# Kernel tuning notes

Measured on AMD Instinct MI355X. Metric: run time of the kernel, lower is better.

The kernel has to match this reference:

```python
import jax, jax.numpy as jnp
import numpy as np

QMIN, QMAX = -128, 127  # int8 range


def _quantize(x, scale, zero_point):
    """Affine quantize float -> int8: clamp(round(x/scale) + zp, -128, 127)."""
    q = jnp.round(x / scale) + zero_point
    return jnp.clip(q, QMIN, QMAX).astype(jnp.int8)


def setup_inputs() -> dict:
    key = jax.random.key(0)
    k1, k2, k3 = jax.random.split(key, 3)
    N, IN, OUT = 8192, 4096, 4096
    inp = jax.random.normal(k1, (N, IN), dtype=jnp.float32)
    # int8 weight table [OUT, IN]
    weight = jax.random.randint(k2, (OUT, IN), QMIN, QMAX + 1, dtype=jnp.int32).astype(jnp.int8)
    # int32 bias [OUT]
    bias = jax.random.randint(k3, (OUT,), -(2 ** 15), 2 ** 15, dtype=jnp.int32)
    return {
        "input": inp,
        "weight": weight,
        "bias": bias,
        "input_scale": 0.02,
        "input_zero_point": 0,
        "output_scale": 4096.0,
        "output_zero_point": 0,
    }


def reference(input, weight, bias, input_scale, input_zero_point, output_scale, output_zero_point):
    # 1) affine quantize input to int8
    q_input = _quantize(input, input_scale, input_zero_point)
    # 2) int32 matmul: F.linear(q_input.int32, weight.int32, bias.int32)
    acc = jnp.matmul(q_input.astype(jnp.int32), weight.astype(jnp.int32).T) + bias  # [N, OUT] int32
    # 3) requantize int32 accumulator to int8 with output scale/zero-point
    q_output = _quantize(acc.astype(jnp.float32), output_scale, output_zero_point)
    return q_output
```

## Files before the change

kernel.cpp:

```cpp
#include <hip/hip_runtime.h>
#include <stdint.h>

typedef int v4i __attribute__((ext_vector_type(4)));
typedef int v16i __attribute__((ext_vector_type(16)));

__device__ __forceinline__ int clamp_i8(int v) {
    return v < -128 ? -128 : (v > 127 ? 127 : v);
}

__device__ __forceinline__ void async_load16(const void* g, void* l) {
    __builtin_amdgcn_global_load_lds(
        (const __attribute__((address_space(1))) void*)g,
        (__attribute__((address_space(3))) void*)l, 16, 0, 0);
}

__global__ void quant_input_kernel(const float4* __restrict__ x, int* __restrict__ q,
                                   const float* __restrict__ scale_p,
                                   const int* __restrict__ zp_p, int n4) {
    const float inv = 1.0f / *scale_p;
    const int zp = *zp_p;
    const int stride = gridDim.x * blockDim.x;
    for (int t = blockIdx.x * blockDim.x + threadIdx.x; t < n4; t += stride) {
        float4 v = x[t];
        int q0 = clamp_i8((int)rintf(v.x * inv) + zp);
        int q1 = clamp_i8((int)rintf(v.y * inv) + zp);
        int q2 = clamp_i8((int)rintf(v.z * inv) + zp);
        int q3 = clamp_i8((int)rintf(v.w * inv) + zp);
        q[t] = (q0 & 255) | ((q1 & 255) << 8) | ((q2 & 255) << 16) | ((q3 & 255) << 24);
    }
}

__global__ void pack_weight_kernel(const int* __restrict__ w, int4* __restrict__ q,
                                   int K, int nfrag) {
    const int stride = gridDim.x * blockDim.x;
    const int Kc32 = K / 32;
    for (int t = blockIdx.x * blockDim.x + threadIdx.x; t < nfrag; t += stride) {
        const int l = t & 63;
        const int rest = t >> 6;
        const int k32 = rest % Kc32;
        const int c32 = rest / Kc32;
        const int col = c32 * 32 + (l & 31);
        const int kb = k32 * 32 + (l >> 5) * 16;
        const int* src = w + (int64_t)col * K + kb;
        int4 out;
        int* op = (int*)&out;
#pragma unroll
        for (int j = 0; j < 4; j++) {
            int4 v = *(const int4*)(src + 4 * j);
            op[j] = (v.x & 255) | ((v.y & 255) << 8) | ((v.z & 255) << 16) | ((v.w & 255) << 24);
        }
        q[t] = out;
    }
}

#define BM 256
#define BN 128
#define BK 64

__global__ __launch_bounds__(256, 2) void gemm_i8_kernel(
    const int8_t* __restrict__ A, const int8_t* __restrict__ W,
    const int* __restrict__ bias, int* __restrict__ C,
    const float* __restrict__ oscale_p, const int* __restrict__ ozp_p,
    int N, int K, int M) {
    __shared__ int8_t lA[2][BM * BK];

    const int tid = threadIdx.x;
    const int lane = tid & 63;
    const int w = tid >> 6;
    const int wm = w >> 1;
    const int wn = w & 1;

    const int bm = blockIdx.y * BM;
    const int bn = blockIdx.x * BN;

    const int s_sub = lane >> 2;
    const int s_col = (((lane & 3) ^ ((s_sub >> 1) & 3))) * 16;
    const int8_t* gA = A + (int64_t)(bm + w * 64 + s_sub) * K + s_col;
    const int64_t rs = (int64_t)16 * K;
    int8_t* lA0 = &lA[0][w * 4096];
    int8_t* lA1 = &lA[1][w * 4096];

    const int Kc32 = K >> 5;
    const int8_t* pB = W + ((int64_t)(blockIdx.x * (BN / 32) + wn * 2) * Kc32 * 64 +
                            lane) * 16;
    const int64_t nsoff = (int64_t)Kc32 * 1024;

    const int m0 = lane & 31;
    const int rsw = (m0 >> 1) & 3;
    const int chi = lane >> 5;

    v16i acc[4][2];
#pragma unroll
    for (int i = 0; i < 4; i++)
#pragma unroll
        for (int j = 0; j < 2; j++)
#pragma unroll
            for (int r = 0; r < 16; r++) acc[i][j][r] = 0;

    v4i bf[2][2];

    {
        async_load16(gA, lA0);
        async_load16(gA + rs, lA0 + 1024);
        async_load16(gA + 2 * rs, lA0 + 2048);
        async_load16(gA + 3 * rs, lA0 + 3072);
        gA += BK;
        bf[0][0] = *(const v4i*)(pB);
        bf[1][0] = *(const v4i*)(pB + 1024);
        bf[0][1] = *(const v4i*)(pB + nsoff);
        bf[1][1] = *(const v4i*)(pB + nsoff + 1024);
        pB += 2048;
    }

    int cur = 0;
    for (int kt = 0; kt < K; kt += BK) {
        __syncthreads();
        const bool more = (kt + BK < K);
        if (more) {
            int8_t* dA = cur ? lA0 : lA1;
            async_load16(gA, dA);
            async_load16(gA + rs, dA + 1024);
            async_load16(gA + 2 * rs, dA + 2048);
            async_load16(gA + 3 * rs, dA + 3072);
            gA += BK;
        }
        const int8_t* cA = &lA[cur][0];
#pragma unroll
        for (int k0 = 0; k0 < BK; k0 += 32) {
            const int cb = k0 >> 4;
            v4i af[4];
#pragma unroll
            for (int ms = 0; ms < 4; ms++)
                af[ms] = *(const v4i*)&cA[(wm * 128 + ms * 32 + m0) * BK +
                                          (((cb + chi) ^ rsw) << 4)];
#pragma unroll
            for (int ms = 0; ms < 4; ms++)
#pragma unroll
                for (int ns = 0; ns < 2; ns++)
                    acc[ms][ns] = __builtin_amdgcn_mfma_i32_32x32x32_i8(
                        af[ms], bf[k0 >> 5][ns], acc[ms][ns], 0, 0, 0);
        }
        if (more) {
            bf[0][0] = *(const v4i*)(pB);
            bf[1][0] = *(const v4i*)(pB + 1024);
            bf[0][1] = *(const v4i*)(pB + nsoff);
            bf[1][1] = *(const v4i*)(pB + nsoff + 1024);
            pB += 2048;
        }
        cur ^= 1;
    }

    const float inv_os = 1.0f / *oscale_p;
    const int ozp = *ozp_p;
    const int rbase = 4 * (lane >> 5);
#pragma unroll
    for (int ns = 0; ns < 2; ns++) {
        const int gn = bn + wn * 64 + ns * 32 + m0;
        const int bv = bias[gn];
#pragma unroll
        for (int ms = 0; ms < 4; ms++) {
            const int gm0 = bm + wm * 128 + ms * 32 + rbase;
            v16i a = acc[ms][ns];
#pragma unroll
            for (int reg = 0; reg < 16; reg++) {
                const int row = (reg & 3) + 8 * (reg >> 2);
                int v = a[reg] + bv;
                int q = (int)rintf((float)v * inv_os) + ozp;
                q = clamp_i8(q);
                C[(int64_t)(gm0 + row) * M + gn] = q;
            }
        }
    }
}

extern "C" void kernel_launch(void* const* d_in, const int* in_sizes, int n_in,
                              void* d_out, int out_size, void* d_ws, size_t ws_size,
                              hipStream_t stream) {
    const float* x = (const float*)d_in[0];
    const int* wgt = (const int*)d_in[1];
    const int* bias = (const int*)d_in[2];
    const float* in_scale = (const float*)d_in[3];
    const int* in_zp = (const int*)d_in[4];
    const float* out_scale = (const float*)d_in[5];
    const int* out_zp = (const int*)d_in[6];

    const int64_t x_elems = (int64_t)in_sizes[0];
    const int OUT = in_sizes[2];
    const int K = in_sizes[1] / OUT;
    const int N = (int)(x_elems / K);

    int8_t* qA = (int8_t*)d_ws;
    int8_t* qW = qA + x_elems;

    {
        int n4 = (int)(x_elems / 4);
        quant_input_kernel<<<4096, 256, 0, stream>>>(
            (const float4*)x, (int*)qA, in_scale, in_zp, n4);
    }
    {
        int nfrag = (int)(((int64_t)OUT * K) / 16);
        pack_weight_kernel<<<2048, 256, 0, stream>>>(
            (const int*)wgt, (int4*)qW, K, nfrag);
    }
    dim3 grid(OUT / BN, N / BM);
    gemm_i8_kernel<<<grid, 256, 0, stream>>>(qA, qW, bias, (int*)d_out,
                                             out_scale, out_zp, N, K, OUT);
}
```

Baseline: 425.1 us.

## Halve GEMM M-tile, raise occupancy, and double-buffer B fragments in registers

```diff
diff --git a/kernel.cpp b/kernel.cpp
--- a/kernel.cpp
+++ b/kernel.cpp
@@ -53,11 +53,11 @@
     }
 }
 
-#define BM 256
+#define BM 128
 #define BN 128
 #define BK 64
 
-__global__ __launch_bounds__(256, 2) void gemm_i8_kernel(
+__global__ __launch_bounds__(256, 3) void gemm_i8_kernel(
     const int8_t* __restrict__ A, const int8_t* __restrict__ W,
     const int* __restrict__ bias, int* __restrict__ C,
     const float* __restrict__ oscale_p, const int* __restrict__ ozp_p,
@@ -75,10 +75,10 @@
 
     const int s_sub = lane >> 2;
     const int s_col = (((lane & 3) ^ ((s_sub >> 1) & 3))) * 16;
-    const int8_t* gA = A + (int64_t)(bm + w * 64 + s_sub) * K + s_col;
+    const int8_t* gA = A + (int64_t)(bm + w * 32 + s_sub) * K + s_col;
     const int64_t rs = (int64_t)16 * K;
-    int8_t* lA0 = &lA[0][w * 4096];
-    int8_t* lA1 = &lA[1][w * 4096];
+    int8_t* lA0 = &lA[0][w * 2048];
+    int8_t* lA1 = &lA[1][w * 2048];
 
     const int Kc32 = K >> 5;
     const int8_t* pB = W + ((int64_t)(blockIdx.x * (BN / 32) + wn * 2) * Kc32 * 64 +
@@ -89,66 +89,64 @@
     const int rsw = (m0 >> 1) & 3;
     const int chi = lane >> 5;
 
-    v16i acc[4][2];
-#pragma unroll
-    for (int i = 0; i < 4; i++)
+    v16i acc[2][2];
+#pragma unroll
+    for (int i = 0; i < 2; i++)
 #pragma unroll
         for (int j = 0; j < 2; j++)
 #pragma unroll
             for (int r = 0; r < 16; r++) acc[i][j][r] = 0;
 
-    v4i bf[2][2];
+    v4i bfA[2][2], bfB[2][2];
 
     {
         async_load16(gA, lA0);
         async_load16(gA + rs, lA0 + 1024);
-        async_load16(gA + 2 * rs, lA0 + 2048);
-        async_load16(gA + 3 * rs, lA0 + 3072);
         gA += BK;
-        bf[0][0] = *(const v4i*)(pB);
-        bf[1][0] = *(const v4i*)(pB + 1024);
-        bf[0][1] = *(const v4i*)(pB + nsoff);
-        bf[1][1] = *(const v4i*)(pB + nsoff + 1024);
+        bfA[0][0] = *(const v4i*)(pB);
+        bfA[1][0] = *(const v4i*)(pB + 1024);
+        bfA[0][1] = *(const v4i*)(pB + nsoff);
+        bfA[1][1] = *(const v4i*)(pB + nsoff + 1024);
         pB += 2048;
     }
 
-    int cur = 0;
-    for (int kt = 0; kt < K; kt += BK) {
-        __syncthreads();
-        const bool more = (kt + BK < K);
-        if (more) {
-            int8_t* dA = cur ? lA0 : lA1;
-            async_load16(gA, dA);
-            async_load16(gA + rs, dA + 1024);
-            async_load16(gA + 2 * rs, dA + 2048);
-            async_load16(gA + 3 * rs, dA + 3072);
-            gA += BK;
-        }
-        const int8_t* cA = &lA[cur][0];
-#pragma unroll
-        for (int k0 = 0; k0 < BK; k0 += 32) {
-            const int cb = k0 >> 4;
-            v4i af[4];
-#pragma unroll
-            for (int ms = 0; ms < 4; ms++)
-                af[ms] = *(const v4i*)&cA[(wm * 128 + ms * 32 + m0) * BK +
-                                          (((cb + chi) ^ rsw) << 4)];
-#pragma unroll
-            for (int ms = 0; ms < 4; ms++)
-#pragma unroll
-                for (int ns = 0; ns < 2; ns++)
-                    acc[ms][ns] = __builtin_amdgcn_mfma_i32_32x32x32_i8(
-                        af[ms], bf[k0 >> 5][ns], acc[ms][ns], 0, 0, 0);
-        }
-        if (more) {
-            bf[0][0] = *(const v4i*)(pB);
-            bf[1][0] = *(const v4i*)(pB + 1024);
-            bf[0][1] = *(const v4i*)(pB + nsoff);
-            bf[1][1] = *(const v4i*)(pB + nsoff + 1024);
-            pB += 2048;
-        }
-        cur ^= 1;
-    }
+#define BODY(CURBUF, BFC, BFN, HASNEXT)                                        \
+    do {                                                                       \
+        __syncthreads();                                                       \
+        if (HASNEXT) {                                                         \
+            int8_t* dA = (CURBUF) ? lA0 : lA1;                                 \
+            async_load16(gA, dA);                                              \
+            async_load16(gA + rs, dA + 1024);                                  \
+            gA += BK;                                                          \
+        }                                                                      \
+        const int8_t* cA = &lA[CURBUF][0];                                     \
+        v4i af[2][2];                                                          \
+        _Pragma("unroll") for (int kh = 0; kh < 2; kh++) {                     \
+            const int cc = (((kh * 2 + chi)) ^ rsw) << 4;                      \
+            _Pragma("unroll") for (int ms = 0; ms < 2; ms++)                   \
+                af[ms][kh] = *(const v4i*)&cA[(wm * 64 + ms * 32 + m0) * BK +  \
+                                              cc];                             \
+        }                                                                      \
+        if (HASNEXT) {                                                         \
+            BFN[0][0] = *(const v4i*)(pB);                                     \
+            BFN[1][0] = *(const v4i*)(pB + 1024);                              \
+            BFN[0][1] = *(const v4i*)(pB + nsoff);                             \
+            BFN[1][1] = *(const v4i*)(pB + nsoff + 1024);                      \
+            pB += 2048;                                                        \
+        }                                                                      \
+        _Pragma("unroll") for (int kh = 0; kh < 2; kh++)                       \
+            _Pragma("unroll") for (int ms = 0; ms < 2; ms++)                   \
+                _Pragma("unroll") for (int ns = 0; ns < 2; ns++)               \
+                    acc[ms][ns] = __builtin_amdgcn_mfma_i32_32x32x32_i8(       \
+                        af[ms][kh], BFC[kh][ns], acc[ms][ns], 0, 0, 0);        \
+    } while (0)
+
+    const int NT = K / BK;
+    for (int t2 = 0; t2 < NT; t2 += 2) {
+        BODY(0, bfA, bfB, true);
+        BODY(1, bfB, bfA, (t2 + 2 < NT));
+    }
+#undef BODY
 
     const float inv_os = 1.0f / *oscale_p;
     const int ozp = *ozp_p;
@@ -158,8 +156,8 @@
         const int gn = bn + wn * 64 + ns * 32 + m0;
         const int bv = bias[gn];
 #pragma unroll
-        for (int ms = 0; ms < 4; ms++) {
-            const int gm0 = bm + wm * 128 + ms * 32 + rbase;
+        for (int ms = 0; ms < 2; ms++) {
+            const int gm0 = bm + wm * 64 + ms * 32 + rbase;
             v16i a = acc[ms][ns];
 #pragma unroll
             for (int reg = 0; reg < 16; reg++) {
```

Result: no change. 429.8 us (+1.1%).

## Pre-pack input into MFMA fragment layout and load both operands directly from global

Applied to the files above, without the earlier changes.

```diff
diff --git a/kernel.cpp b/kernel.cpp
--- a/kernel.cpp
+++ b/kernel.cpp
@@ -8,25 +8,33 @@
     return v < -128 ? -128 : (v > 127 ? 127 : v);
 }
 
-__device__ __forceinline__ void async_load16(const void* g, void* l) {
-    __builtin_amdgcn_global_load_lds(
-        (const __attribute__((address_space(1))) void*)g,
-        (__attribute__((address_space(3))) void*)l, 16, 0, 0);
-}
-
-__global__ void quant_input_kernel(const float4* __restrict__ x, int* __restrict__ q,
+__global__ void quant_input_kernel(const float* __restrict__ x, int4* __restrict__ q,
                                    const float* __restrict__ scale_p,
-                                   const int* __restrict__ zp_p, int n4) {
+                                   const int* __restrict__ zp_p, int K, int nfrag) {
     const float inv = 1.0f / *scale_p;
     const int zp = *zp_p;
+    const int Kc32 = K / 32;
     const int stride = gridDim.x * blockDim.x;
-    for (int t = blockIdx.x * blockDim.x + threadIdx.x; t < n4; t += stride) {
-        float4 v = x[t];
-        int q0 = clamp_i8((int)rintf(v.x * inv) + zp);
-        int q1 = clamp_i8((int)rintf(v.y * inv) + zp);
-        int q2 = clamp_i8((int)rintf(v.z * inv) + zp);
-        int q3 = clamp_i8((int)rintf(v.w * inv) + zp);
-        q[t] = (q0 & 255) | ((q1 & 255) << 8) | ((q2 & 255) << 16) | ((q3 & 255) << 24);
+    for (int t = blockIdx.x * blockDim.x + threadIdx.x; t < nfrag; t += stride) {
+        const int l = t & 63;
+        const int rest = t >> 6;
+        const int k32 = rest % Kc32;
+        const int r32 = rest / Kc32;
+        const int row = r32 * 32 + (l & 31);
+        const int kb = k32 * 32 + (l >> 5) * 16;
+        const float* src = x + (int64_t)row * K + kb;
+        int4 out;
+        int* op = (int*)&out;
+#pragma unroll
+        for (int j = 0; j < 4; j++) {
+            float4 v = *(const float4*)(src + 4 * j);
+            int q0 = clamp_i8((int)rintf(v.x * inv) + zp);
+            int q1 = clamp_i8((int)rintf(v.y * inv) + zp);
+            int q2 = clamp_i8((int)rintf(v.z * inv) + zp);
+            int q3 = clamp_i8((int)rintf(v.w * inv) + zp);
+            op[j] = (q0 & 255) | ((q1 & 255) << 8) | ((q2 & 255) << 16) | ((q3 & 255) << 24);
+        }
+        q[t] = out;
     }
 }
 
@@ -54,102 +62,89 @@
 }
 
 #define BM 256
-#define BN 128
+#define BN 256
 #define BK 64
 
-__global__ __launch_bounds__(256, 2) void gemm_i8_kernel(
+__global__ __launch_bounds__(512, 2) void gemm_i8_kernel(
     const int8_t* __restrict__ A, const int8_t* __restrict__ W,
     const int* __restrict__ bias, int* __restrict__ C,
     const float* __restrict__ oscale_p, const int* __restrict__ ozp_p,
     int N, int K, int M) {
-    __shared__ int8_t lA[2][BM * BK];
-
     const int tid = threadIdx.x;
     const int lane = tid & 63;
     const int w = tid >> 6;
-    const int wm = w >> 1;
-    const int wn = w & 1;
-
-    const int bm = blockIdx.y * BM;
-    const int bn = blockIdx.x * BN;
-
-    const int s_sub = lane >> 2;
-    const int s_col = (((lane & 3) ^ ((s_sub >> 1) & 3))) * 16;
-    const int8_t* gA = A + (int64_t)(bm + w * 64 + s_sub) * K + s_col;
-    const int64_t rs = (int64_t)16 * K;
-    int8_t* lA0 = &lA[0][w * 4096];
-    int8_t* lA1 = &lA[1][w * 4096];
+    const int wm = w >> 2;
+    const int wn = w & 3;
+
+    const int nwg = gridDim.x;
+    const int mblocks = M / BN;
+    int bid = blockIdx.x;
+    if ((nwg & 7) == 0) bid = (bid & 7) * (nwg >> 3) + (bid >> 3);
+    const int by = bid / mblocks;
+    const int bx = bid % mblocks;
+    const int bm = by * BM;
+    const int bn = bx * BN;
 
     const int Kc32 = K >> 5;
-    const int8_t* pB = W + ((int64_t)(blockIdx.x * (BN / 32) + wn * 2) * Kc32 * 64 +
-                            lane) * 16;
-    const int64_t nsoff = (int64_t)Kc32 * 1024;
+
+    const int8_t* pA[4];
+#pragma unroll
+    for (int ms = 0; ms < 4; ms++) {
+        const int r32 = (bm >> 5) + wm * 4 + ms;
+        pA[ms] = A + ((int64_t)r32 * Kc32 * 64 + lane) * 16;
+    }
+    const int8_t* pB[2];
+#pragma unroll
+    for (int ns = 0; ns < 2; ns++) {
+        const int c32 = (bn >> 5) + wn * 2 + ns;
+        pB[ns] = W + ((int64_t)c32 * Kc32 * 64 + lane) * 16;
+    }
+
+    v16i acc[4][2];
+#pragma unroll
+    for (int i = 0; i < 4; i++)
+#pragma unroll
+        for (int j = 0; j < 2; j++)
+#pragma unroll
+            for (int r = 0; r < 16; r++) acc[i][j][r] = 0;
+
+    v4i af[4][2], bf[2][2];
+
+#define LOADF                                                   \
+    do {                                                        \
+        _Pragma("unroll") for (int ms = 0; ms < 4; ms++) {      \
+            af[ms][0] = *(const v4i*)(pA[ms]);                  \
+            af[ms][1] = *(const v4i*)(pA[ms] + 1024);           \
+            pA[ms] += 2048;                                     \
+        }                                                       \
+        _Pragma("unroll") for (int ns = 0; ns < 2; ns++) {      \
+            bf[ns][0] = *(const v4i*)(pB[ns]);                  \
+            bf[ns][1] = *(const v4i*)(pB[ns] + 1024);           \
+            pB[ns] += 2048;                                     \
+        }                                                       \
+    } while (0)
+
+#define MFMA_ALL                                                              \
+    do {                                                                      \
+        _Pragma("unroll") for (int ms = 0; ms < 4; ms++)                      \
+            _Pragma("unroll") for (int ns = 0; ns < 2; ns++)                  \
+                _Pragma("unroll") for (int kh = 0; kh < 2; kh++)              \
+                    acc[ms][ns] = __builtin_amdgcn_mfma_i32_32x32x32_i8(      \
+                        af[ms][kh], bf[ns][kh], acc[ms][ns], 0, 0, 0);        \
+    } while (0)
+
+    const int NT = K / BK;
+    LOADF;
+    for (int kt = 0; kt < NT - 1; ++kt) {
+        MFMA_ALL;
+        LOADF;
+    }
+    MFMA_ALL;
+
+#undef LOADF
+#undef MFMA_ALL
 
     const int m0 = lane & 31;
-    const int rsw = (m0 >> 1) & 3;
-    const int chi = lane >> 5;
-
-    v16i acc[4][2];
-#pragma unroll
-    for (int i = 0; i < 4; i++)
-#pragma unroll
-        for (int j = 0; j < 2; j++)
-#pragma unroll
-            for (int r = 0; r < 16; r++) acc[i][j][r] = 0;
-
-    v4i bf[2][2];
-
-    {
-        async_load16(gA, lA0);
-        async_load16(gA + rs, lA0 + 1024);
-        async_load16(gA + 2 * rs, lA0 + 2048);
-        async_load16(gA + 3 * rs, lA0 + 3072);
-        gA += BK;
-        bf[0][0] = *(const v4i*)(pB);
-        bf[1][0] = *(const v4i*)(pB + 1024);
-        bf[0][1] = *(const v4i*)(pB + nsoff);
-        bf[1][1] = *(const v4i*)(pB + nsoff + 1024);
-        pB += 2048;
-    }
-
-    int cur = 0;
-    for (int kt = 0; kt < K; kt += BK) {
-        __syncthreads();
-        const bool more = (kt + BK < K);
-        if (more) {
-            int8_t* dA = cur ? lA0 : lA1;
-            async_load16(gA, dA);
-            async_load16(gA + rs, dA + 1024);
-            async_load16(gA + 2 * rs, dA + 2048);
-            async_load16(gA + 3 * rs, dA + 3072);
-            gA += BK;
-        }
-        const int8_t* cA = &lA[cur][0];
-#pragma unroll
-        for (int k0 = 0; k0 < BK; k0 += 32) {
-            const int cb = k0 >> 4;
-            v4i af[4];
-#pragma unroll
-            for (int ms = 0; ms < 4; ms++)
-                af[ms] = *(const v4i*)&cA[(wm * 128 + ms * 32 + m0) * BK +
-                                          (((cb + chi) ^ rsw) << 4)];
-#pragma unroll
-            for (int ms = 0; ms < 4; ms++)
-#pragma unroll
-                for (int ns = 0; ns < 2; ns++)
-                    acc[ms][ns] = __builtin_amdgcn_mfma_i32_32x32x32_i8(
-                        af[ms], bf[k0 >> 5][ns], acc[ms][ns], 0, 0, 0);
-        }
-        if (more) {
-            bf[0][0] = *(const v4i*)(pB);
-            bf[1][0] = *(const v4i*)(pB + 1024);
-            bf[0][1] = *(const v4i*)(pB + nsoff);
-            bf[1][1] = *(const v4i*)(pB + nsoff + 1024);
-            pB += 2048;
-        }
-        cur ^= 1;
-    }
-
     const float inv_os = 1.0f / *oscale_p;
     const int ozp = *ozp_p;
     const int rbase = 4 * (lane >> 5);
@@ -193,16 +188,16 @@
     int8_t* qW = qA + x_elems;
 
     {
-        int n4 = (int)(x_elems / 4);
+        int nfrag = (int)(x_elems / 16);
         quant_input_kernel<<<4096, 256, 0, stream>>>(
-            (const float4*)x, (int*)qA, in_scale, in_zp, n4);
+            x, (int4*)qA, in_scale, in_zp, K, nfrag);
     }
     {
         int nfrag = (int)(((int64_t)OUT * K) / 16);
         pack_weight_kernel<<<2048, 256, 0, stream>>>(
             (const int*)wgt, (int4*)qW, K, nfrag);
     }
-    dim3 grid(OUT / BN, N / BM);
-    gemm_i8_kernel<<<grid, 256, 0, stream>>>(qA, qW, bias, (int*)d_out,
-                                             out_scale, out_zp, N, K, OUT);
-}
+    const int nblocks = (OUT / BN) * (N / BM);
+    gemm_i8_kernel<<<dim3(nblocks), 512, 0, stream>>>(
+        qA, qW, bias, (int*)d_out, out_scale, out_zp, N, K, OUT);
+}
```

Measured after the change: 436.9 us. 1.03x slower.
